# Kernel tuning notes

Hardware: AMD Instinct MI355X
Metric: run time of the kernel (lower is better)

The kernel has to match this reference:

```python
import jax, jax.numpy as jnp
import numpy as np

N_NODES = 50000
NEG_SLOPE = 0.2


def gat_conv(x, src, dst, W, att_src, att_dst, bias, concat):
    # x: [N, F_in], W: [H*D, F_in], att_*: [H, D], bias: [H*D] or [D]
    N = x.shape[0]
    H, D = att_src.shape
    h = (x @ W.T).reshape(N, H, D)                      # [N, H, D]
    a_src = jnp.einsum('nhd,hd->nh', h, att_src)        # [N, H]
    a_dst = jnp.einsum('nhd,hd->nh', h, att_dst)        # [N, H]
    e = jax.nn.leaky_relu(a_src[src] + a_dst[dst], NEG_SLOPE)  # [E, H]
    # softmax over incoming edges of each destination node
    m = jax.ops.segment_max(e, dst, num_segments=N)     # [N, H]
    ex = jnp.exp(e - m[dst])
    denom = jax.ops.segment_sum(ex, dst, num_segments=N)
    alpha = ex / denom[dst]                             # [E, H]
    msg = alpha[:, :, None] * h[src]                    # [E, H, D]
    out = jax.ops.segment_sum(msg, dst, num_segments=N) # [N, H, D]
    out = out.reshape(N, H * D) if concat else out.mean(axis=1)
    return out + bias


def setup_inputs() -> dict:
    key = jax.random.key(0)
    ks = jax.random.split(key, 10)
    nfeat, nhid, nclass, heads = 256, 128, 40, 4
    d1 = nhid // heads  # 32
    E = 800000
    x = jax.random.normal(ks[0], (N_NODES, nfeat), dtype=jnp.float32)
    edge_index = jax.random.randint(ks[1], (2, E), 0, N_NODES, dtype=jnp.int64)
    s = 0.1
    W1 = jax.random.normal(ks[2], (heads * d1, nfeat), dtype=jnp.float32) * s
    att_src1 = jax.random.normal(ks[3], (heads, d1), dtype=jnp.float32) * s
    att_dst1 = jax.random.normal(ks[4], (heads, d1), dtype=jnp.float32) * s
    b1 = jnp.zeros((heads * d1,), dtype=jnp.float32)
    W2 = jax.random.normal(ks[5], (nclass, nhid), dtype=jnp.float32) * s
    att_src2 = jax.random.normal(ks[6], (1, nclass), dtype=jnp.float32) * s
    att_dst2 = jax.random.normal(ks[7], (1, nclass), dtype=jnp.float32) * s
    b2 = jnp.zeros((nclass,), dtype=jnp.float32)
    return {"x": x, "edge_index": edge_index, "W1": W1, "att_src1": att_src1,
            "att_dst1": att_dst1, "b1": b1, "W2": W2, "att_src2": att_src2,
            "att_dst2": att_dst2, "b2": b2}


def reference(x, edge_index, W1, att_src1, att_dst1, b1, W2, att_src2, att_dst2, b2):
    # PyG GATConv adds self-loops by default
    loops = jnp.arange(N_NODES, dtype=edge_index.dtype)
    src = jnp.concatenate([edge_index[0], loops])
    dst = jnp.concatenate([edge_index[1], loops])
    h = gat_conv(x, src, dst, W1, att_src1, att_dst1, b1, concat=True)
    h = jax.nn.relu(h)
    # dropout is identity in eval mode
    out = gat_conv(h, src, dst, W2, att_src2, att_dst2, b2, concat=True)
    return out
```

## Files before the change

kernel.cpp:

```cpp
#include <hip/hip_runtime.h>
#include <hip/hip_bf16.h>
#include <cstdint>
#include <cstddef>

#define N_NODES 50000
#define NEG_SLOPE 0.2f
#define NB 196
#define BIN_CHUNK 8192
#define SLICE_MAX 14336

typedef float floatx4 __attribute__((ext_vector_type(4)));
typedef short shortx8 __attribute__((ext_vector_type(8)));

__device__ __forceinline__ unsigned short f2b(float f) {
    union { float f; unsigned u; } v; v.f = f;
    unsigned u = v.u;
    return (unsigned short)((u + 0x7FFFu + ((u >> 16) & 1u)) >> 16);
}
__device__ __forceinline__ float b2f(unsigned short b) {
    union { unsigned u; float f; } v; v.u = ((unsigned)b) << 16;
    return v.f;
}

__global__ __launch_bounds__(256) void bucket_hist_kernel(
    const int* __restrict__ ei, int E0, int E, int* __restrict__ bhist) {
    __shared__ int h[NB];
    int t = threadIdx.x;
    for (int i = t; i < NB; i += 256) h[i] = 0;
    __syncthreads();
    int base = blockIdx.x * BIN_CHUNK;
    int end = min(base + BIN_CHUNK, E);
    for (int e = base + t; e < end; e += 256) {
        int d = (e < E0) ? ei[E0 + e] : (e - E0);
        atomicAdd(&h[d >> 8], 1);
    }
    __syncthreads();
    for (int i = t; i < NB; i += 256)
        if (h[i]) atomicAdd(&bhist[i], h[i]);
}

__global__ __launch_bounds__(256) void bucket_scan_kernel(
    const int* __restrict__ bhist, int* __restrict__ bbase,
    int* __restrict__ bcursor, int* __restrict__ rowptr, int E) {
    __shared__ int buf[256];
    int t = threadIdx.x;
    int v = (t < NB) ? bhist[t] : 0;
    int x = v;
    for (int off = 1; off < 256; off <<= 1) {
        buf[t] = x; __syncthreads();
        int y = (t >= off) ? buf[t - off] : 0;
        __syncthreads();
        x += y;
    }
    if (t < NB) {
        bbase[t] = x - v;
        bcursor[t] = x - v;
    }
    if (t == NB - 1) bbase[NB] = x;
    if (t == 0) rowptr[N_NODES] = E;
}

__global__ __launch_bounds__(256) void bin_kernel(
    const int* __restrict__ ei, int E0, int E,
    int* __restrict__ bcursor, unsigned int* __restrict__ ebuf) {
    __shared__ int h[NB];
    __shared__ int gbase[NB];
    int t = threadIdx.x;
    for (int i = t; i < NB; i += 256) h[i] = 0;
    __syncthreads();
    int base = blockIdx.x * BIN_CHUNK;
    int end = min(base + BIN_CHUNK, E);
    for (int e = base + t; e < end; e += 256) {
        int d = (e < E0) ? ei[E0 + e] : (e - E0);
        atomicAdd(&h[d >> 8], 1);
    }
    __syncthreads();
    for (int i = t; i < NB; i += 256) {
        int c = h[i];
        gbase[i] = c ? atomicAdd(&bcursor[i], c) : 0;
        h[i] = 0;
    }
    __syncthreads();
    for (int e = base + t; e < end; e += 256) {
        int s, d;
        if (e < E0) { s = ei[e]; d = ei[E0 + e]; }
        else        { s = e - E0; d = e - E0; }
        int b = d >> 8;
        int off = atomicAdd(&h[b], 1);
        ebuf[gbase[b] + off] = (unsigned)s | ((unsigned)(d & 255) << 16);
    }
}

__global__ __launch_bounds__(256) void build_kernel(
    const unsigned int* __restrict__ ebuf, const int* __restrict__ bbase,
    int* __restrict__ rowptr, int* __restrict__ csr_src,
    unsigned short* __restrict__ csr_dst) {
    __shared__ int h[256];
    __shared__ int lrp[257];
    __shared__ unsigned int stag[SLICE_MAX];
    int b = blockIdx.x, t = threadIdx.x;
    int e0 = bbase[b], e1 = bbase[b + 1];
    int cnt = e1 - e0;
    int n0 = b << 8;
    h[t] = 0;
    __syncthreads();
    for (int i = t; i < cnt; i += 256)
        atomicAdd(&h[ebuf[e0 + i] >> 16], 1);
    __syncthreads();
    int v = h[t], x = v;
    __shared__ int buf[256];
    for (int off = 1; off < 256; off <<= 1) {
        buf[t] = x; __syncthreads();
        int y = (t >= off) ? buf[t - off] : 0;
        __syncthreads();
        x += y;
    }
    lrp[t] = x - v;
    if (t == 255) lrp[256] = x;
    h[t] = 0;
    __syncthreads();
    int n = n0 + t;
    if (n < N_NODES) rowptr[n] = e0 + lrp[t];
    for (int i = t; i < cnt; i += 256) {
        unsigned int v2 = ebuf[e0 + i];
        int dloc = v2 >> 16;
        int off = atomicAdd(&h[dloc], 1);
        stag[lrp[dloc] + off] = v2;
    }
    __syncthreads();
    for (int i = t; i < cnt; i += 256) {
        unsigned int v2 = stag[i];
        csr_src[e0 + i] = (int)(v2 & 0xFFFFu);
        csr_dst[e0 + i] = (unsigned short)(n0 + (v2 >> 16));
    }
}

__global__ __launch_bounds__(256) void edge_w1_kernel(
    const int* __restrict__ csr_src, const unsigned short* __restrict__ csr_dst,
    const float* __restrict__ a_src, const float* __restrict__ a_dst,
    float* __restrict__ ew, int E) {
    int e = blockIdx.x * blockDim.x + threadIdx.x;
    if (e >= E) return;
    int s = csr_src[e];
    int d = csr_dst[e];
    float4 as = *(const float4*)&a_src[s << 2];
    float4 ad = *(const float4*)&a_dst[d << 2];
    float4 w;
    float l;
    l = as.x + ad.x; l = l > 0.f ? l : NEG_SLOPE * l; w.x = __expf(l);
    l = as.y + ad.y; l = l > 0.f ? l : NEG_SLOPE * l; w.y = __expf(l);
    l = as.z + ad.z; l = l > 0.f ? l : NEG_SLOPE * l; w.z = __expf(l);
    l = as.w + ad.w; l = l > 0.f ? l : NEG_SLOPE * l; w.w = __expf(l);
    *(float4*)&ew[(size_t)e << 2] = w;
}

__global__ __launch_bounds__(256) void edge_w2_kernel(
    const int* __restrict__ csr_src, const unsigned short* __restrict__ csr_dst,
    const float* __restrict__ a_src, const float* __restrict__ a_dst,
    float* __restrict__ ew, int E) {
    int e = blockIdx.x * blockDim.x + threadIdx.x;
    if (e >= E) return;
    float l = a_src[csr_src[e]] + a_dst[csr_dst[e]];
    l = l > 0.f ? l : NEG_SLOPE * l;
    ew[e] = __expf(l);
}

template <int BM, int BN, int NREAL, int KK, typename InT, typename OutT>
__global__ __launch_bounds__(256) void gemm_bf16_kernel(
    const InT* __restrict__ A, const float* __restrict__ B,
    OutT* __restrict__ C, int M) {
    const int BK = 64, LDK = 72;
    const int NT = BN / 16;
    __shared__ unsigned short As[BM * LDK];
    __shared__ unsigned short Bs[BN * LDK];
    const int t = threadIdx.x;
    const int wave = t >> 6, lane = t & 63;
    const int lrow = lane & 15, lkg = lane >> 4;
    const int bm = blockIdx.x * BM;

    floatx4 acc[NT] = {};

    for (int k0 = 0; k0 < KK; k0 += BK) {
        __syncthreads();
        if constexpr (sizeof(InT) == 4) {
            for (int i = t; i < BM * 16; i += 256) {
                int r = i >> 4, c4 = (i & 15) << 2;
                int gr = bm + r;
                float4 v = make_float4(0.f, 0.f, 0.f, 0.f);
                if (gr < M) v = *(const float4*)&A[(size_t)gr * KK + k0 + c4];
                int o = r * LDK + c4;
                As[o] = f2b(v.x); As[o + 1] = f2b(v.y);
                As[o + 2] = f2b(v.z); As[o + 3] = f2b(v.w);
            }
        } else {
            for (int i = t; i < BM * 8; i += 256) {
                int r = i >> 3, c8 = (i & 7) << 3;
                int gr = bm + r;
                shortx8 v = {};
                if (gr < M) v = *(const shortx8*)&A[(size_t)gr * KK + k0 + c8];
                *(shortx8*)&As[r * LDK + c8] = v;
            }
        }
        for (int i = t; i < BN * 16; i += 256) {
            int r = i >> 4, c4 = (i & 15) << 2;
            float4 v = make_float4(0.f, 0.f, 0.f, 0.f);
            if (r < NREAL) v = *(const float4*)&B[(size_t)r * KK + k0 + c4];
            int o = r * LDK + c4;
            Bs[o] = f2b(v.x); Bs[o + 1] = f2b(v.y);
            Bs[o + 2] = f2b(v.z); Bs[o + 3] = f2b(v.w);
        }
        __syncthreads();

        for (int ks = 0; ks < BK; ks += 32) {
            int kc = ks + lkg * 8;
            int row = wave * 16 + lrow;
            shortx8 a = *(const shortx8*)&As[row * LDK + kc];
#pragma unroll
            for (int nt = 0; nt < NT; nt++) {
                shortx8 b = *(const shortx8*)&Bs[(nt * 16 + lrow) * LDK + kc];
                acc[nt] = __builtin_amdgcn_mfma_f32_16x16x32_bf16(a, b, acc[nt], 0, 0, 0);
            }
        }
    }
#pragma unroll
    for (int nt = 0; nt < NT; nt++)
#pragma unroll
        for (int r = 0; r < 4; r++) {
            int row = bm + wave * 16 + lkg * 4 + r;
            int col = nt * 16 + lrow;
            if (row < M && col < NREAL) {
                if constexpr (sizeof(OutT) == 2)
                    C[(size_t)row * NREAL + col] = f2b(acc[nt][r]);
                else
                    C[(size_t)row * NREAL + col] = acc[nt][r];
            }
        }
}

__global__ void att1_kernel(const unsigned short* __restrict__ h1b,
                            const float* __restrict__ att_src,
                            const float* __restrict__ att_dst,
                            float* __restrict__ a_src, float* __restrict__ a_dst,
                            int N) {
    int i = blockIdx.x * blockDim.x + threadIdx.x;
    if (i >= N * 4) return;
    int h = i & 3;
    const ushort4* hp = (const ushort4*)(h1b + (size_t)i * 32);
    const float4* as = (const float4*)(att_src + h * 32);
    const float4* ad = (const float4*)(att_dst + h * 32);
    float ssum = 0.f, dsum = 0.f;
#pragma unroll
    for (int j = 0; j < 8; j++) {
        ushort4 hv = hp[j];
        float4 av = as[j], dv = ad[j];
        float x0 = b2f(hv.x), x1 = b2f(hv.y), x2 = b2f(hv.z), x3 = b2f(hv.w);
        ssum += x0 * av.x + x1 * av.y + x2 * av.z + x3 * av.w;
        dsum += x0 * dv.x + x1 * dv.y + x2 * dv.z + x3 * dv.w;
    }
    a_src[i] = ssum;
    a_dst[i] = dsum;
}

__global__ void att2_kernel(const unsigned short* __restrict__ h2b,
                            const float* __restrict__ att_src,
                            const float* __restrict__ att_dst,
                            float* __restrict__ a_src, float* __restrict__ a_dst,
                            int N) {
    int n = blockIdx.x * blockDim.x + threadIdx.x;
    if (n >= N) return;
    const ushort4* hp = (const ushort4*)(h2b + (size_t)n * 40);
    const float4* as = (const float4*)att_src;
    const float4* ad = (const float4*)att_dst;
    float ssum = 0.f, dsum = 0.f;
#pragma unroll
    for (int j = 0; j < 10; j++) {
        ushort4 hv = hp[j];
        float4 av = as[j], dv = ad[j];
        float x0 = b2f(hv.x), x1 = b2f(hv.y), x2 = b2f(hv.z), x3 = b2f(hv.w);
        ssum += x0 * av.x + x1 * av.y + x2 * av.z + x3 * av.w;
        dsum += x0 * dv.x + x1 * dv.y + x2 * dv.z + x3 * dv.w;
    }
    a_src[n] = ssum;
    a_dst[n] = dsum;
}

__global__ __launch_bounds__(256) void agg1_kernel(
    const unsigned short* __restrict__ h1b, const float* __restrict__ ew,
    const int* __restrict__ rowptr, const int* __restrict__ csr_src,
    const float* __restrict__ b1, unsigned short* __restrict__ zb, int N) {
    int wave = threadIdx.x >> 6, lane = threadIdx.x & 63;
    int n = blockIdx.x * 4 + wave;
    if (n >= N) return;
    int q = lane >> 4, sub = lane & 15, headq = sub >> 2;
    int beg = rowptr[n], deg = rowptr[n + 1] - beg;

    floatx4 a0 = {0.f, 0.f, 0.f, 0.f}, a1 = {0.f, 0.f, 0.f, 0.f};
    float den = 0.f;
    for (int c0 = 0; c0 < deg; c0 += 16) {
        int idx = c0 + (lane >> 2);
        int s_e = (idx < deg) ? csr_src[beg + idx] : 0;
        float w_e = (idx < deg) ? ew[((size_t)(beg + c0) << 2) + lane] : 0.f;
#pragma unroll
        for (int i = 0; i < 4; i++) {
            int eb = 4 * i + q;
            int s = __shfl(s_e, eb << 2);
            float w = __shfl(w_e, (eb << 2) + headq);
            shortx8 v = *(const shortx8*)&h1b[((size_t)s << 7) + (sub << 3)];
            den += w;
            a0.x += w * b2f((unsigned short)v[0]);
            a0.y += w * b2f((unsigned short)v[1]);
            a0.z += w * b2f((unsigned short)v[2]);
            a0.w += w * b2f((unsigned short)v[3]);
            a1.x += w * b2f((unsigned short)v[4]);
            a1.y += w * b2f((unsigned short)v[5]);
            a1.z += w * b2f((unsigned short)v[6]);
            a1.w += w * b2f((unsigned short)v[7]);
        }
    }
#pragma unroll
    for (int off = 16; off <= 32; off <<= 1) {
        a0.x += __shfl_xor(a0.x, off); a0.y += __shfl_xor(a0.y, off);
        a0.z += __shfl_xor(a0.z, off); a0.w += __shfl_xor(a0.w, off);
        a1.x += __shfl_xor(a1.x, off); a1.y += __shfl_xor(a1.y, off);
        a1.z += __shfl_xor(a1.z, off); a1.w += __shfl_xor(a1.w, off);
        den  += __shfl_xor(den, off);
    }
    if (q == 0) {
        float inv = 1.f / den;
        float4 bb0 = *(const float4*)&b1[sub << 3];
        float4 bb1 = *(const float4*)&b1[(sub << 3) + 4];
        shortx8 r;
        r[0] = (short)f2b(fmaxf(a0.x * inv + bb0.x, 0.f));
        r[1] = (short)f2b(fmaxf(a0.y * inv + bb0.y, 0.f));
        r[2] = (short)f2b(fmaxf(a0.z * inv + bb0.z, 0.f));
        r[3] = (short)f2b(fmaxf(a0.w * inv + bb0.w, 0.f));
        r[4] = (short)f2b(fmaxf(a1.x * inv + bb1.x, 0.f));
        r[5] = (short)f2b(fmaxf(a1.y * inv + bb1.y, 0.f));
        r[6] = (short)f2b(fmaxf(a1.z * inv + bb1.z, 0.f));
        r[7] = (short)f2b(fmaxf(a1.w * inv + bb1.w, 0.f));
        *(shortx8*)&zb[((size_t)n << 7) + (sub << 3)] = r;
    }
}

__global__ __launch_bounds__(256) void agg2_kernel(
    const unsigned short* __restrict__ h2b, const float* __restrict__ ew,
    const int* __restrict__ rowptr, const int* __restrict__ csr_src,
    const float* __restrict__ b2, float* __restrict__ out, int N) {
    int wave = threadIdx.x >> 6, lane = threadIdx.x & 63;
    int n = blockIdx.x * 4 + wave;
    if (n >= N) return;
    int half = lane >> 5, pos = lane & 31;
    int beg = rowptr[n], deg = rowptr[n + 1] - beg;

    float2 acc = {0.f, 0.f};
    float den = 0.f;
    for (int c0 = 0; c0 < deg; c0 += 32) {
        int idx = c0 + (lane & 31);
        int s_e = (idx < deg) ? csr_src[beg + idx] : 0;
        float w_e = (idx < deg) ? ew[beg + idx] : 0.f;
#pragma unroll
        for (int e = 0; e < 32; e += 2) {
            int el = e + half;
            int s = __shfl(s_e, el);
            float w = __shfl(w_e, el);
            den += w;
            if (pos < 20) {
                ushort2 v = *(const ushort2*)&h2b[(size_t)s * 40 + pos * 2];
                acc.x += w * b2f(v.x);
                acc.y += w * b2f(v.y);
            }
        }
    }
    acc.x += __shfl_xor(acc.x, 32);
    acc.y += __shfl_xor(acc.y, 32);
    den   += __shfl_xor(den, 32);
    if (half == 0 && pos < 20) {
        float inv = 1.f / den;
        float2 bb = *(const float2*)&b2[pos * 2];
        float2 o;
        o.x = acc.x * inv + bb.x;
        o.y = acc.y * inv + bb.y;
        *(float2*)&out[(size_t)n * 40 + pos * 2] = o;
    }
}

extern "C" void kernel_launch(void* const* d_in, const int* in_sizes, int n_in,
                              void* d_out, int out_size, void* d_ws, size_t ws_size,
                              hipStream_t stream) {
    const float* x        = (const float*)d_in[0];
    const int*   ei       = (const int*)d_in[1];
    const float* W1       = (const float*)d_in[2];
    const float* att_src1 = (const float*)d_in[3];
    const float* att_dst1 = (const float*)d_in[4];
    const float* b1       = (const float*)d_in[5];
    const float* W2       = (const float*)d_in[6];
    const float* att_src2 = (const float*)d_in[7];
    const float* att_dst2 = (const float*)d_in[8];
    const float* b2       = (const float*)d_in[9];
    float* out = (float*)d_out;

    const int N  = N_NODES;
    const int E0 = in_sizes[1] / 2;
    const int E  = E0 + N;
    const int NBLK = (E + BIN_CHUNK - 1) / BIN_CHUNK;

    char* ws = (char*)d_ws;
    unsigned short* h1b = (unsigned short*)(ws + 0);
    unsigned short* zb  = (unsigned short*)(ws + 12800000);
    unsigned short* h2b = (unsigned short*)(ws + 25600000);
    float* a_src1 = (float*)(ws + 29600000);
    float* a_dst1 = (float*)(ws + 30400000);
    float* a_src2 = (float*)(ws + 31200000);
    float* a_dst2 = (float*)(ws + 31400000);
    int*   rowptr = (int*)(ws + 31600000);
    int*   bhist  = (int*)(ws + 31800192);
    int*   bbase  = (int*)(ws + 31801088);
    int*   bcursor= (int*)(ws + 31801984);
    unsigned int* ebuf = (unsigned int*)(ws + 31802880);
    int*   csr_src= (int*)(ws + 35202880);
    unsigned short* csr_dst = (unsigned short*)(ws + 38602880);
    float* ew1    = (float*)(ws + 40302880);
    float* ew2    = (float*)(ws + 53902880);

    hipMemsetAsync(bhist, 0, NB * sizeof(int), stream);

    bucket_hist_kernel<<<NBLK, 256, 0, stream>>>(ei, E0, E, bhist);
    bucket_scan_kernel<<<1, 256, 0, stream>>>(bhist, bbase, bcursor, rowptr, E);
    bin_kernel<<<NBLK, 256, 0, stream>>>(ei, E0, E, bcursor, ebuf);
    build_kernel<<<NB, 256, 0, stream>>>(ebuf, bbase, rowptr, csr_src, csr_dst);

    gemm_bf16_kernel<64, 128, 128, 256, float, unsigned short>
        <<<(N + 63) / 64, 256, 0, stream>>>(x, W1, h1b, N);
    att1_kernel<<<(N * 4 + 255) / 256, 256, 0, stream>>>(h1b, att_src1, att_dst1, a_src1, a_dst1, N);
    edge_w1_kernel<<<(E + 255) / 256, 256, 0, stream>>>(csr_src, csr_dst, a_src1, a_dst1, ew1, E);
    agg1_kernel<<<(N + 3) / 4, 256, 0, stream>>>(h1b, ew1, rowptr, csr_src, b1, zb, N);

    gemm_bf16_kernel<64, 48, 40, 128, unsigned short, unsigned short>
        <<<(N + 63) / 64, 256, 0, stream>>>(zb, W2, h2b, N);
    att2_kernel<<<(N + 255) / 256, 256, 0, stream>>>(h2b, att_src2, att_dst2, a_src2, a_dst2, N);
    edge_w2_kernel<<<(E + 255) / 256, 256, 0, stream>>>(csr_src, csr_dst, a_src2, a_dst2, ew2, E);
    agg2_kernel<<<(N + 3) / 4, 256, 0, stream>>>(h2b, ew2, rowptr, csr_src, b2, out, N);
}
```

Measured before the change: 273.1 us.

## Split layer-1 features and edge weights head-major; aggregate one head per block

The first GEMM now writes h1 in a head-major layout ([head][node][32]) and edge weights are stored per head in separate planes. agg1 runs four times as many blocks, each handling one head, so the gather table per pass is a quarter of the size and more likely to stay in L2. agg2 is also reworked to process 4 edges per wave with 4-wide loads. The cost is narrower 4-byte gathers in agg1 and the CSR index/rowptr being read four times.

```diff
diff --git a/kernel.cpp b/kernel.cpp
--- a/kernel.cpp
+++ b/kernel.cpp
@@ -8,6 +8,7 @@
 #define NB 196
 #define BIN_CHUNK 8192
 #define SLICE_MAX 14336
+#define NBLK1 12500
 
 typedef float floatx4 __attribute__((ext_vector_type(4)));
 typedef short shortx8 __attribute__((ext_vector_type(8)));
@@ -145,13 +146,11 @@
     int d = csr_dst[e];
     float4 as = *(const float4*)&a_src[s << 2];
     float4 ad = *(const float4*)&a_dst[d << 2];
-    float4 w;
     float l;
-    l = as.x + ad.x; l = l > 0.f ? l : NEG_SLOPE * l; w.x = __expf(l);
-    l = as.y + ad.y; l = l > 0.f ? l : NEG_SLOPE * l; w.y = __expf(l);
-    l = as.z + ad.z; l = l > 0.f ? l : NEG_SLOPE * l; w.z = __expf(l);
-    l = as.w + ad.w; l = l > 0.f ? l : NEG_SLOPE * l; w.w = __expf(l);
-    *(float4*)&ew[(size_t)e << 2] = w;
+    l = as.x + ad.x; l = l > 0.f ? l : NEG_SLOPE * l; ew[e]         = __expf(l);
+    l = as.y + ad.y; l = l > 0.f ? l : NEG_SLOPE * l; ew[E + e]     = __expf(l);
+    l = as.z + ad.z; l = l > 0.f ? l : NEG_SLOPE * l; ew[2 * E + e] = __expf(l);
+    l = as.w + ad.w; l = l > 0.f ? l : NEG_SLOPE * l; ew[3 * E + e] = __expf(l);
 }
 
 __global__ __launch_bounds__(256) void edge_w2_kernel(
@@ -165,7 +164,7 @@
     ew[e] = __expf(l);
 }
 
-template <int BM, int BN, int NREAL, int KK, typename InT, typename OutT>
+template <int BM, int BN, int NREAL, int KK, typename InT, typename OutT, bool HM>
 __global__ __launch_bounds__(256) void gemm_bf16_kernel(
     const InT* __restrict__ A, const float* __restrict__ B,
     OutT* __restrict__ C, int M) {
@@ -229,10 +228,14 @@
             int row = bm + wave * 16 + lkg * 4 + r;
             int col = nt * 16 + lrow;
             if (row < M && col < NREAL) {
-                if constexpr (sizeof(OutT) == 2)
+                if constexpr (HM) {
+                    C[(size_t)(col >> 5) * ((size_t)N_NODES * 32)
+                      + (size_t)row * 32 + (col & 31)] = f2b(acc[nt][r]);
+                } else if constexpr (sizeof(OutT) == 2) {
                     C[(size_t)row * NREAL + col] = f2b(acc[nt][r]);
-                else
+                } else {
                     C[(size_t)row * NREAL + col] = acc[nt][r];
+                }
             }
         }
 }
@@ -244,8 +247,8 @@
                             int N) {
     int i = blockIdx.x * blockDim.x + threadIdx.x;
     if (i >= N * 4) return;
-    int h = i & 3;
-    const ushort4* hp = (const ushort4*)(h1b + (size_t)i * 32);
+    int h = i & 3, n = i >> 2;
+    const ushort4* hp = (const ushort4*)(h1b + (size_t)h * N * 32 + (size_t)n * 32);
     const float4* as = (const float4*)(att_src + h * 32);
     const float4* ad = (const float4*)(att_dst + h * 32);
     float ssum = 0.f, dsum = 0.f;
@@ -287,58 +290,47 @@
 __global__ __launch_bounds__(256) void agg1_kernel(
     const unsigned short* __restrict__ h1b, const float* __restrict__ ew,
     const int* __restrict__ rowptr, const int* __restrict__ csr_src,
-    const float* __restrict__ b1, unsigned short* __restrict__ zb, int N) {
+    const float* __restrict__ b1, unsigned short* __restrict__ zb,
+    int N, int E) {
     int wave = threadIdx.x >> 6, lane = threadIdx.x & 63;
-    int n = blockIdx.x * 4 + wave;
+    int head = blockIdx.x / NBLK1, nb = blockIdx.x % NBLK1;
+    int n = nb * 4 + wave;
     if (n >= N) return;
-    int q = lane >> 4, sub = lane & 15, headq = sub >> 2;
+    int q = lane >> 4, sub = lane & 15;
     int beg = rowptr[n], deg = rowptr[n + 1] - beg;
-
-    floatx4 a0 = {0.f, 0.f, 0.f, 0.f}, a1 = {0.f, 0.f, 0.f, 0.f};
+    const unsigned short* tab = h1b + (size_t)head * N * 32;
+    const float* ewh = ew + (size_t)head * E;
+
+    float2 acc = {0.f, 0.f};
     float den = 0.f;
     for (int c0 = 0; c0 < deg; c0 += 16) {
-        int idx = c0 + (lane >> 2);
+        int idx = c0 + (lane & 15);
         int s_e = (idx < deg) ? csr_src[beg + idx] : 0;
-        float w_e = (idx < deg) ? ew[((size_t)(beg + c0) << 2) + lane] : 0.f;
+        float w_e = (idx < deg) ? ewh[beg + idx] : 0.f;
 #pragma unroll
         for (int i = 0; i < 4; i++) {
             int eb = 4 * i + q;
-            int s = __shfl(s_e, eb << 2);
-            float w = __shfl(w_e, (eb << 2) + headq);
-            shortx8 v = *(const shortx8*)&h1b[((size_t)s << 7) + (sub << 3)];
+            int s = __shfl(s_e, eb);
+            float w = __shfl(w_e, eb);
+            ushort2 v = *(const ushort2*)&tab[(size_t)s * 32 + (sub << 1)];
             den += w;
-            a0.x += w * b2f((unsigned short)v[0]);
-            a0.y += w * b2f((unsigned short)v[1]);
-            a0.z += w * b2f((unsigned short)v[2]);
-            a0.w += w * b2f((unsigned short)v[3]);
-            a1.x += w * b2f((unsigned short)v[4]);
-            a1.y += w * b2f((unsigned short)v[5]);
-            a1.z += w * b2f((unsigned short)v[6]);
-            a1.w += w * b2f((unsigned short)v[7]);
+            acc.x += w * b2f(v.x);
+            acc.y += w * b2f(v.y);
         }
     }
 #pragma unroll
     for (int off = 16; off <= 32; off <<= 1) {
-        a0.x += __shfl_xor(a0.x, off); a0.y += __shfl_xor(a0.y, off);
-        a0.z += __shfl_xor(a0.z, off); a0.w += __shfl_xor(a0.w, off);
-        a1.x += __shfl_xor(a1.x, off); a1.y += __shfl_xor(a1.y, off);
-        a1.z += __shfl_xor(a1.z, off); a1.w += __shfl_xor(a1.w, off);
-        den  += __shfl_xor(den, off);
+        acc.x += __shfl_xor(acc.x, off);
+        acc.y += __shfl_xor(acc.y, off);
+        den   += __shfl_xor(den, off);
     }
     if (q == 0) {
         float inv = 1.f / den;
-        float4 bb0 = *(const float4*)&b1[sub << 3];
-        float4 bb1 = *(const float4*)&b1[(sub << 3) + 4];
-        shortx8 r;
-        r[0] = (short)f2b(fmaxf(a0.x * inv + bb0.x, 0.f));
-        r[1] = (short)f2b(fmaxf(a0.y * inv + bb0.y, 0.f));
-        r[2] = (short)f2b(fmaxf(a0.z * inv + bb0.z, 0.f));
-        r[3] = (short)f2b(fmaxf(a0.w * inv + bb0.w, 0.f));
-        r[4] = (short)f2b(fmaxf(a1.x * inv + bb1.x, 0.f));
-        r[5] = (short)f2b(fmaxf(a1.y * inv + bb1.y, 0.f));
-        r[6] = (short)f2b(fmaxf(a1.z * inv + bb1.z, 0.f));
-        r[7] = (short)f2b(fmaxf(a1.w * inv + bb1.w, 0.f));
-        *(shortx8*)&zb[((size_t)n << 7) + (sub << 3)] = r;
+        float2 bb = *(const float2*)&b1[(head << 5) + (sub << 1)];
+        ushort2 r;
+        r.x = f2b(fmaxf(acc.x * inv + bb.x, 0.f));
+        r.y = f2b(fmaxf(acc.y * inv + bb.y, 0.f));
+        *(ushort2*)&zb[((size_t)n << 7) + (head << 5) + (sub << 1)] = r;
     }
 }
 
@@ -349,38 +341,45 @@
     int wave = threadIdx.x >> 6, lane = threadIdx.x & 63;
     int n = blockIdx.x * 4 + wave;
     if (n >= N) return;
-    int half = lane >> 5, pos = lane & 31;
+    int q = lane >> 4, sub = lane & 15;
     int beg = rowptr[n], deg = rowptr[n + 1] - beg;
 
-    float2 acc = {0.f, 0.f};
+    floatx4 acc = {0.f, 0.f, 0.f, 0.f};
     float den = 0.f;
-    for (int c0 = 0; c0 < deg; c0 += 32) {
-        int idx = c0 + (lane & 31);
+    for (int c0 = 0; c0 < deg; c0 += 16) {
+        int idx = c0 + (lane & 15);
         int s_e = (idx < deg) ? csr_src[beg + idx] : 0;
         float w_e = (idx < deg) ? ew[beg + idx] : 0.f;
 #pragma unroll
-        for (int e = 0; e < 32; e += 2) {
-            int el = e + half;
-            int s = __shfl(s_e, el);
-            float w = __shfl(w_e, el);
+        for (int i = 0; i < 4; i++) {
+            int eb = 4 * i + q;
+            int s = __shfl(s_e, eb);
+            float w = __shfl(w_e, eb);
             den += w;
-            if (pos < 20) {
-                ushort2 v = *(const ushort2*)&h2b[(size_t)s * 40 + pos * 2];
+            if (sub < 10) {
+                ushort4 v = *(const ushort4*)&h2b[(size_t)s * 40 + (sub << 2)];
                 acc.x += w * b2f(v.x);
                 acc.y += w * b2f(v.y);
+                acc.z += w * b2f(v.z);
+                acc.w += w * b2f(v.w);
             }
         }
     }
-    acc.x += __shfl_xor(acc.x, 32);
-    acc.y += __shfl_xor(acc.y, 32);
-    den   += __shfl_xor(den, 32);
-    if (half == 0 && pos < 20) {
+#pragma unroll
+    for (int off = 16; off <= 32; off <<= 1) {
+        acc.x += __shfl_xor(acc.x, off); acc.y += __shfl_xor(acc.y, off);
+        acc.z += __shfl_xor(acc.z, off); acc.w += __shfl_xor(acc.w, off);
+        den   += __shfl_xor(den, off);
+    }
+    if (q == 0 && sub < 10) {
         float inv = 1.f / den;
-        float2 bb = *(const float2*)&b2[pos * 2];
-        float2 o;
+        float4 bb = *(const float4*)&b2[sub << 2];
+        float4 o;
         o.x = acc.x * inv + bb.x;
         o.y = acc.y * inv + bb.y;
-        *(float2*)&out[(size_t)n * 40 + pos * 2] = o;
+        o.z = acc.z * inv + bb.z;
+        o.w = acc.w * inv + bb.w;
+        *(float4*)&out[(size_t)n * 40 + (sub << 2)] = o;
     }
 }
 
@@ -429,13 +428,13 @@
     bin_kernel<<<NBLK, 256, 0, stream>>>(ei, E0, E, bcursor, ebuf);
     build_kernel<<<NB, 256, 0, stream>>>(ebuf, bbase, rowptr, csr_src, csr_dst);
 
-    gemm_bf16_kernel<64, 128, 128, 256, float, unsigned short>
+    gemm_bf16_kernel<64, 128, 128, 256, float, unsigned short, true>
         <<<(N + 63) / 64, 256, 0, stream>>>(x, W1, h1b, N);
     att1_kernel<<<(N * 4 + 255) / 256, 256, 0, stream>>>(h1b, att_src1, att_dst1, a_src1, a_dst1, N);
     edge_w1_kernel<<<(E + 255) / 256, 256, 0, stream>>>(csr_src, csr_dst, a_src1, a_dst1, ew1, E);
-    agg1_kernel<<<(N + 3) / 4, 256, 0, stream>>>(h1b, ew1, rowptr, csr_src, b1, zb, N);
-
-    gemm_bf16_kernel<64, 48, 40, 128, unsigned short, unsigned short>
+    agg1_kernel<<<4 * NBLK1, 256, 0, stream>>>(h1b, ew1, rowptr, csr_src, b1, zb, N, E);
+
+    gemm_bf16_kernel<64, 48, 40, 128, unsigned short, unsigned short, false>
         <<<(N + 63) / 64, 256, 0, stream>>>(zb, W2, h2b, N);
     att2_kernel<<<(N + 255) / 256, 256, 0, stream>>>(h2b, att_src2, att_dst2, a_src2, a_dst2, N);
     edge_w2_kernel<<<(E + 255) / 256, 256, 0, stream>>>(csr_src, csr_dst, a_src2, a_dst2, ew2, E);
```

After: 295.1 us. 1.08x slower.
